# Kernel tuning notes

Hardware: AMD Instinct MI355X
Metric: run time of the kernel (lower is better)

## Reference

```python
import jax, jax.numpy as jnp
import numpy as np


def a_powers(A, t):
    # A: [K, n, n]; returns [t, K, n, n] = stack(I, A, A^2, ..., A^(t-1))
    K, n, _ = A.shape
    result = jnp.broadcast_to(jnp.eye(n, dtype=A.dtype), (1, K, n, n))
    lift = A
    while result.shape[0] < t:
        result = jnp.concatenate([result, result @ lift], axis=0)
        lift = lift @ lift
    return result[:t]


def fast_conv_real(a, b):
    # a: [len1, K, n, n], b: [batch, len2, K, n] -> conv(b, a): [batch, len1+len2-1, K, n]
    len1 = a.shape[0]
    len2 = b.shape[1]
    T = 2 ** int(np.ceil(np.log2(len1 + len2 - 1)))
    Af = jnp.fft.rfft(a, n=T, axis=0)
    Bf = jnp.fft.rfft(b, n=T, axis=1)
    Cf = jnp.einsum('blki,lkij->blkj', Bf, Af)
    c = jnp.fft.irfft(Cf, n=T, axis=1)
    return c[:, :len1 + len2 - 1]


def setup_inputs() -> dict:
    key = jax.random.key(0)
    k_u, k_x0, k_theta, k_B, k_C = jax.random.split(key, 5)
    batch, length = 8, 4096
    input_size, state_size, output_size = 256, 256, 256
    blk = 2
    K = state_size // blk  # 128
    u = jax.random.normal(k_u, (batch, length, input_size), dtype=jnp.float32)
    x0 = jax.random.normal(k_x0, (batch, K, blk), dtype=jnp.float32)
    # A initialized as K random 2x2 rotation blocks (as in __init__)
    theta = 2 * jnp.pi * jax.random.uniform(k_theta, (K,), dtype=jnp.float32)
    c, s = jnp.cos(theta), jnp.sin(theta)
    A = jnp.stack([jnp.stack([c, s], -1), jnp.stack([-s, c], -1)], -2)  # [K, 2, 2]
    B = jax.random.normal(k_B, (input_size, state_size), dtype=jnp.float32) / (state_size + input_size) ** 0.5
    C = jax.random.normal(k_C, (state_size, output_size), dtype=jnp.float32) / (state_size + output_size) ** 0.5
    return {"u": u, "x0": x0, "A": A, "B": B, "C": C}


def reference(u, x0, A, B, C):
    batch, length, _ = u.shape
    K, blk, _ = A.shape
    Aps = a_powers(A, length + 1)          # [length+1, K, blk, blk]
    uB = (u @ B).reshape(batch, length, K, blk)
    x = fast_conv_real(Aps[:-1], uB)[:, :length]  # [batch, length, K, blk]
    x = x + jnp.einsum('bki,lkij->blkj', x0, Aps[1:])
    new_state = x[:, -1]                    # [batch, K, blk]
    y = x.reshape(batch, length, K * blk) @ C
    return (y, new_state)
```

## Files before the change

### kernel.cpp

```cpp
#include <hip/hip_runtime.h>
#include <hip/hip_bf16.h>

typedef __bf16 bf16x2_t __attribute__((ext_vector_type(2)));
typedef __bf16 bf16x8_t __attribute__((ext_vector_type(8)));
typedef float f32x4 __attribute__((ext_vector_type(4)));

#define BATCH   8
#define LENGTH  4096
#define KHALF   128
#define MTOT    (BATCH*LENGTH)
#define NCHUNK  128
#define LC      32

#define SWZ(ch, row) ((ch) ^ ((row) & 7))

__global__ __launch_bounds__(256) void transpose_bc(
    const float* __restrict__ Bsrc, const float* __restrict__ Csrc,
    __bf16* __restrict__ BT, __bf16* __restrict__ CT) {
  const float* src = blockIdx.y ? Csrc : Bsrc;
  __bf16* dst      = blockIdx.y ? CT   : BT;
  int n  = blockIdx.x;
  int kk = threadIdx.x;
  dst[n * 256 + kk] = (__bf16)src[kk * 256 + n];
}

__global__ __launch_bounds__(256) void gemm1_fused(
    const float* __restrict__ u, const __bf16* __restrict__ BT,
    const float* __restrict__ Aarr,
    __bf16* __restrict__ uB, float2* __restrict__ P) {
  __shared__ __align__(16) __bf16 sA[64 * 256];

  const int tid  = threadIdx.x;
  const int lane = tid & 63;
  const int wave = tid >> 6;
  const int m_l  = lane & 15, quad = lane >> 4;
  const int m0   = blockIdx.x * 64;
  const int b    = m0 >> 12;
  const int t0   = m0 & 4095;

#pragma unroll
  for (int i = 0; i < 8; ++i) {
    int s   = tid + i * 256;
    int row = s >> 5, ch = s & 31;
    const float4* g = (const float4*)(u + (size_t)(m0 + row) * 256 + ch * 8);
    float4 a = g[0], c = g[1];
    bf16x8_t v;
    v[0]=(__bf16)a.x; v[1]=(__bf16)a.y; v[2]=(__bf16)a.z; v[3]=(__bf16)a.w;
    v[4]=(__bf16)c.x; v[5]=(__bf16)c.y; v[6]=(__bf16)c.z; v[7]=(__bf16)c.w;
    *(bf16x8_t*)&sA[row * 256 + SWZ(ch, row) * 8] = v;
  }
  __syncthreads();

  f32x4 acc[4][4];
#pragma unroll
  for (int mi = 0; mi < 4; ++mi)
#pragma unroll
    for (int ni = 0; ni < 4; ++ni)
#pragma unroll
      for (int r = 0; r < 4; ++r) acc[mi][ni][r] = 0.f;

#pragma unroll
  for (int kc8 = 0; kc8 < 8; ++kc8) {
    bf16x8_t af[4], bfr[4];
#pragma unroll
    for (int mi = 0; mi < 4; ++mi) {
      int row = mi * 16 + m_l;
      int c   = kc8 * 4 + quad;
      af[mi] = *(const bf16x8_t*)&sA[row * 256 + SWZ(c, row) * 8];
    }
#pragma unroll
    for (int ni = 0; ni < 4; ++ni) {
      int n = wave * 64 + ni * 16 + m_l;
      bfr[ni] = *(const bf16x8_t*)(BT + (size_t)n * 256 + kc8 * 32 + quad * 8);
    }
#pragma unroll
    for (int mi = 0; mi < 4; ++mi)
#pragma unroll
      for (int ni = 0; ni < 4; ++ni)
        acc[mi][ni] = __builtin_amdgcn_mfma_f32_16x16x32_bf16(af[mi], bfr[ni], acc[mi][ni], 0, 0, 0);
  }
  __syncthreads();

  __bf16* sT = sA;
#pragma unroll
  for (int mi = 0; mi < 4; ++mi)
#pragma unroll
    for (int ni = 0; ni < 4; ++ni)
#pragma unroll
      for (int r = 0; r < 4; ++r) {
        int row = mi * 16 + quad * 4 + r;
        int col = wave * 64 + ni * 16 + m_l;
        sT[row * 256 + SWZ(col >> 3, row) * 8 + (col & 7)] = (__bf16)acc[mi][ni][r];
      }
  __syncthreads();

#pragma unroll
  for (int i = 0; i < 8; ++i) {
    int s   = tid + i * 256;
    int row = s >> 5, ch = s & 31;
    *(bf16x8_t*)(uB + (size_t)(m0 + row) * 256 + ch * 8) =
        *(const bf16x8_t*)&sT[row * 256 + SWZ(ch, row) * 8];
  }

  {
    int k   = tid & 127;
    int chl = tid >> 7;
    float cc = Aarr[4 * k], sv = Aarr[4 * k + 1];
    float hr = 0.f, hi = 0.f;
#pragma unroll 8
    for (int j = 0; j < LC; ++j) {
      int row = chl * 32 + j;
      bf16x2_t v2 = *(const bf16x2_t*)&sT[row * 256 + SWZ(k >> 2, row) * 8 + ((2 * k) & 7)];
      float t = fmaf(hr, cc, fmaf(-hi, sv, (float)v2[0]));
      hi      = fmaf(hr, sv, fmaf( hi, cc, (float)v2[1]));
      hr = t;
    }
    int chg = (t0 >> 5) + chl;
    P[((size_t)b * NCHUNK + chg) * KHALF + k] = make_float2(hr, hi);
  }
}

__global__ __launch_bounds__(256) void scan_carry2(
    const float* __restrict__ Aarr, const float* __restrict__ x0,
    const float2* __restrict__ P, float2* __restrict__ H,
    float* __restrict__ state_out) {
  const int lane = threadIdx.x & 63;
  const int wv   = threadIdx.x >> 6;
  const int p    = blockIdx.x * 4 + wv;
  const int b    = p >> 7, k = p & 127;
  const float cc = Aarr[4 * k], sv = Aarr[4 * k + 1];

  float wr = cc, wi = sv;
#pragma unroll
  for (int i = 0; i < 5; ++i) { float nr = wr*wr - wi*wi; wi = 2.f*wr*wi; wr = nr; }
  float Wr[6], Wi[6];
  Wr[0] = wr*wr - wi*wi; Wi[0] = 2.f*wr*wi;
#pragma unroll
  for (int s = 1; s < 6; ++s) { Wr[s] = Wr[s-1]*Wr[s-1] - Wi[s-1]*Wi[s-1]; Wi[s] = 2.f*Wr[s-1]*Wi[s-1]; }

  float2 P0 = P[((size_t)b * NCHUNK + 2 * lane)     * KHALF + k];
  float2 P1 = P[((size_t)b * NCHUNK + 2 * lane + 1) * KHALF + k];
  float qr = fmaf(wr, P0.x, fmaf(-wi, P0.y, P1.x));
  float qi = fmaf(wr, P0.y, fmaf( wi, P0.x, P1.y));
  float Sr = qr, Si = qi;
#pragma unroll
  for (int s = 0; s < 6; ++s) {
    float tr = __shfl_up(Sr, 1 << s, 64);
    float ti = __shfl_up(Si, 1 << s, 64);
    if (lane >= (1 << s)) {
      float nSr = fmaf(Wr[s], tr, fmaf(-Wi[s], ti, Sr));
      float nSi = fmaf(Wr[s], ti, fmaf( Wi[s], tr, Si));
      Sr = nSr; Si = nSi;
    }
  }
  float Ar = __shfl_up(Sr, 1, 64), Ai = __shfl_up(Si, 1, 64);
  if (lane == 0) { Ar = 0.f; Ai = 0.f; }
  float pr = 1.f, pi = 0.f;
#pragma unroll
  for (int s = 0; s < 6; ++s)
    if ((lane >> s) & 1) { float nr = pr*Wr[s] - pi*Wi[s]; pi = pr*Wi[s] + pi*Wr[s]; pr = nr; }

  float x0r = x0[b * 256 + 2 * k], x0i = x0[b * 256 + 2 * k + 1];
  float H0r = fmaf(pr, x0r, fmaf(-pi, x0i, Ar));
  float H0i = fmaf(pr, x0i, fmaf( pi, x0r, Ai));
  H[((size_t)b * NCHUNK + 2 * lane) * KHALF + k] = make_float2(H0r, H0i);
  float H1r = fmaf(wr, H0r, fmaf(-wi, H0i, P0.x));
  float H1i = fmaf(wr, H0i, fmaf( wi, H0r, P0.y));
  H[((size_t)b * NCHUNK + 2 * lane + 1) * KHALF + k] = make_float2(H1r, H1i);
  if (lane == 63) {
    state_out[b * 256 + 2 * k]     = fmaf(wr, H1r, fmaf(-wi, H1i, P1.x));
    state_out[b * 256 + 2 * k + 1] = fmaf(wr, H1i, fmaf( wi, H1r, P1.y));
  }
}

__global__ __launch_bounds__(256) void gemm2_fused(
    const __bf16* __restrict__ uB, const float* __restrict__ Aarr,
    const float2* __restrict__ H, const __bf16* __restrict__ CT,
    float* __restrict__ Y) {
  __shared__ __align__(16) __bf16 sX[64 * 256];

  const int tid  = threadIdx.x;
  const int lane = tid & 63;
  const int wave = tid >> 6;
  const int m_l  = lane & 15, quad = lane >> 4;
  const int m0   = blockIdx.x * 64;
  const int b    = m0 >> 12;
  const int t0   = m0 & 4095;

#pragma unroll
  for (int i = 0; i < 8; ++i) {
    int s   = tid + i * 256;
    int row = s >> 5, ch = s & 31;
    *(bf16x8_t*)&sX[row * 256 + SWZ(ch, row) * 8] =
        *(const bf16x8_t*)(uB + (size_t)(m0 + row) * 256 + ch * 8);
  }
  __syncthreads();

  {
    int k   = tid & 127;
    int chl = tid >> 7;
    float cc = Aarr[4 * k], sv = Aarr[4 * k + 1];
    float2 h = H[((size_t)b * NCHUNK + (t0 >> 5) + chl) * KHALF + k];
    float hr = h.x, hi = h.y;
#pragma unroll 8
    for (int j = 0; j < LC; ++j) {
      int row = chl * 32 + j;
      int idx = row * 256 + SWZ(k >> 2, row) * 8 + ((2 * k) & 7);
      bf16x2_t v2 = *(const bf16x2_t*)&sX[idx];
      float t = fmaf(hr, cc, fmaf(-hi, sv, (float)v2[0]));
      hi      = fmaf(hr, sv, fmaf( hi, cc, (float)v2[1]));
      hr = t;
      bf16x2_t o; o[0] = (__bf16)hr; o[1] = (__bf16)hi;
      *(bf16x2_t*)&sX[idx] = o;
    }
  }
  __syncthreads();

  f32x4 acc[4][4];
#pragma unroll
  for (int mi = 0; mi < 4; ++mi)
#pragma unroll
    for (int ni = 0; ni < 4; ++ni)
#pragma unroll
      for (int r = 0; r < 4; ++r) acc[mi][ni][r] = 0.f;

#pragma unroll
  for (int kc8 = 0; kc8 < 8; ++kc8) {
    bf16x8_t af[4], bfr[4];
#pragma unroll
    for (int mi = 0; mi < 4; ++mi) {
      int row = mi * 16 + m_l;
      int c   = kc8 * 4 + quad;
      af[mi] = *(const bf16x8_t*)&sX[row * 256 + SWZ(c, row) * 8];
    }
#pragma unroll
    for (int ni = 0; ni < 4; ++ni) {
      int n = wave * 64 + ni * 16 + m_l;
      bfr[ni] = *(const bf16x8_t*)(CT + (size_t)n * 256 + kc8 * 32 + quad * 8);
    }
#pragma unroll
    for (int mi = 0; mi < 4; ++mi)
#pragma unroll
      for (int ni = 0; ni < 4; ++ni)
        acc[mi][ni] = __builtin_amdgcn_mfma_f32_16x16x32_bf16(af[mi], bfr[ni], acc[mi][ni], 0, 0, 0);
  }

#pragma unroll
  for (int mi = 0; mi < 4; ++mi)
#pragma unroll
    for (int ni = 0; ni < 4; ++ni)
#pragma unroll
      for (int r = 0; r < 4; ++r) {
        int row = m0 + mi * 16 + quad * 4 + r;
        int col = wave * 64 + ni * 16 + m_l;
        Y[(size_t)row * 256 + col] = acc[mi][ni][r];
      }
}

extern "C" void kernel_launch(void* const* d_in, const int* in_sizes, int n_in,
                              void* d_out, int out_size, void* d_ws, size_t ws_size,
                              hipStream_t stream) {
  const float* u  = (const float*)d_in[0];
  const float* x0 = (const float*)d_in[1];
  const float* A  = (const float*)d_in[2];
  const float* B  = (const float*)d_in[3];
  const float* C  = (const float*)d_in[4];

  float* y         = (float*)d_out;
  float* state_out = y + (size_t)MTOT * 256;

  char* ws = (char*)d_ws;
  __bf16* BT = (__bf16*)ws;  ws += 256 * 256 * 2;
  __bf16* CT = (__bf16*)ws;  ws += 256 * 256 * 2;
  __bf16* uB = (__bf16*)ws;  ws += (size_t)MTOT * 256 * 2;
  float2* P  = (float2*)ws;  ws += (size_t)BATCH * NCHUNK * KHALF * sizeof(float2);
  float2* H  = (float2*)ws;  ws += (size_t)BATCH * NCHUNK * KHALF * sizeof(float2);

  transpose_bc<<<dim3(256, 2), 256, 0, stream>>>(B, C, BT, CT);
  gemm1_fused<<<dim3(MTOT / 64), 256, 0, stream>>>(u, BT, A, uB, P);
  scan_carry2<<<dim3(256), 256, 0, stream>>>(A, x0, P, H, state_out);
  gemm2_fused<<<dim3(MTOT / 64), 256, 0, stream>>>(uB, A, H, CT, y);
}
```

Baseline: 119.2 us.

## Fuse chunk-carry scan into gemm2 by serially recomputing each chunk's prefix

Drops the separate scan_carry2 kernel and the H buffer. Each gemm2_fused thread now rebuilds its chunk's starting state by stepping from x0 through every preceding chunk partial in P, using A^32. The thread on the final chunk also writes new_state. This saves one kernel launch and the H write/read round trip. In exchange, each thread runs a serial loop of up to 127 dependent complex FMAs and P loads, which adds a lot of redundant L2 traffic and latency before the GEMM starts.

```diff
diff --git a/kernel.cpp b/kernel.cpp
--- a/kernel.cpp
+++ b/kernel.cpp
@@ -120,63 +120,11 @@
   }
 }
 
-__global__ __launch_bounds__(256) void scan_carry2(
-    const float* __restrict__ Aarr, const float* __restrict__ x0,
-    const float2* __restrict__ P, float2* __restrict__ H,
-    float* __restrict__ state_out) {
-  const int lane = threadIdx.x & 63;
-  const int wv   = threadIdx.x >> 6;
-  const int p    = blockIdx.x * 4 + wv;
-  const int b    = p >> 7, k = p & 127;
-  const float cc = Aarr[4 * k], sv = Aarr[4 * k + 1];
-
-  float wr = cc, wi = sv;
-#pragma unroll
-  for (int i = 0; i < 5; ++i) { float nr = wr*wr - wi*wi; wi = 2.f*wr*wi; wr = nr; }
-  float Wr[6], Wi[6];
-  Wr[0] = wr*wr - wi*wi; Wi[0] = 2.f*wr*wi;
-#pragma unroll
-  for (int s = 1; s < 6; ++s) { Wr[s] = Wr[s-1]*Wr[s-1] - Wi[s-1]*Wi[s-1]; Wi[s] = 2.f*Wr[s-1]*Wi[s-1]; }
-
-  float2 P0 = P[((size_t)b * NCHUNK + 2 * lane)     * KHALF + k];
-  float2 P1 = P[((size_t)b * NCHUNK + 2 * lane + 1) * KHALF + k];
-  float qr = fmaf(wr, P0.x, fmaf(-wi, P0.y, P1.x));
-  float qi = fmaf(wr, P0.y, fmaf( wi, P0.x, P1.y));
-  float Sr = qr, Si = qi;
-#pragma unroll
-  for (int s = 0; s < 6; ++s) {
-    float tr = __shfl_up(Sr, 1 << s, 64);
-    float ti = __shfl_up(Si, 1 << s, 64);
-    if (lane >= (1 << s)) {
-      float nSr = fmaf(Wr[s], tr, fmaf(-Wi[s], ti, Sr));
-      float nSi = fmaf(Wr[s], ti, fmaf( Wi[s], tr, Si));
-      Sr = nSr; Si = nSi;
-    }
-  }
-  float Ar = __shfl_up(Sr, 1, 64), Ai = __shfl_up(Si, 1, 64);
-  if (lane == 0) { Ar = 0.f; Ai = 0.f; }
-  float pr = 1.f, pi = 0.f;
-#pragma unroll
-  for (int s = 0; s < 6; ++s)
-    if ((lane >> s) & 1) { float nr = pr*Wr[s] - pi*Wi[s]; pi = pr*Wi[s] + pi*Wr[s]; pr = nr; }
-
-  float x0r = x0[b * 256 + 2 * k], x0i = x0[b * 256 + 2 * k + 1];
-  float H0r = fmaf(pr, x0r, fmaf(-pi, x0i, Ar));
-  float H0i = fmaf(pr, x0i, fmaf( pi, x0r, Ai));
-  H[((size_t)b * NCHUNK + 2 * lane) * KHALF + k] = make_float2(H0r, H0i);
-  float H1r = fmaf(wr, H0r, fmaf(-wi, H0i, P0.x));
-  float H1i = fmaf(wr, H0i, fmaf( wi, H0r, P0.y));
-  H[((size_t)b * NCHUNK + 2 * lane + 1) * KHALF + k] = make_float2(H1r, H1i);
-  if (lane == 63) {
-    state_out[b * 256 + 2 * k]     = fmaf(wr, H1r, fmaf(-wi, H1i, P1.x));
-    state_out[b * 256 + 2 * k + 1] = fmaf(wr, H1i, fmaf( wi, H1r, P1.y));
-  }
-}
-
 __global__ __launch_bounds__(256) void gemm2_fused(
     const __bf16* __restrict__ uB, const float* __restrict__ Aarr,
-    const float2* __restrict__ H, const __bf16* __restrict__ CT,
-    float* __restrict__ Y) {
+    const float2* __restrict__ P, const float* __restrict__ x0,
+    const __bf16* __restrict__ CT, float* __restrict__ Y,
+    float* __restrict__ state_out) {
   __shared__ __align__(16) __bf16 sX[64 * 256];
 
   const int tid  = threadIdx.x;
@@ -199,9 +147,21 @@
   {
     int k   = tid & 127;
     int chl = tid >> 7;
+    int chg = (t0 >> 5) + chl;
     float cc = Aarr[4 * k], sv = Aarr[4 * k + 1];
-    float2 h = H[((size_t)b * NCHUNK + (t0 >> 5) + chl) * KHALF + k];
-    float hr = h.x, hi = h.y;
+
+    float wr = cc, wi = sv;
+#pragma unroll
+    for (int i = 0; i < 5; ++i) { float nr = wr*wr - wi*wi; wi = 2.f*wr*wi; wr = nr; }
+
+    float hr = x0[b * 256 + 2 * k], hi = x0[b * 256 + 2 * k + 1];
+    for (int j = 0; j < chg; ++j) {
+      float2 pj = P[((size_t)b * NCHUNK + j) * KHALF + k];
+      float t = fmaf(wr, hr, fmaf(-wi, hi, pj.x));
+      hi      = fmaf(wr, hi, fmaf( wi, hr, pj.y));
+      hr = t;
+    }
+
 #pragma unroll 8
     for (int j = 0; j < LC; ++j) {
       int row = chl * 32 + j;
@@ -213,6 +173,11 @@
       bf16x2_t o; o[0] = (__bf16)hr; o[1] = (__bf16)hi;
       *(bf16x2_t*)&sX[idx] = o;
     }
+
+    if (chg == NCHUNK - 1) {
+      state_out[b * 256 + 2 * k]     = hr;
+      state_out[b * 256 + 2 * k + 1] = hi;
+    }
   }
   __syncthreads();
 
@@ -274,10 +239,8 @@
   __bf16* CT = (__bf16*)ws;  ws += 256 * 256 * 2;
   __bf16* uB = (__bf16*)ws;  ws += (size_t)MTOT * 256 * 2;
   float2* P  = (float2*)ws;  ws += (size_t)BATCH * NCHUNK * KHALF * sizeof(float2);
-  float2* H  = (float2*)ws;  ws += (size_t)BATCH * NCHUNK * KHALF * sizeof(float2);
 
   transpose_bc<<<dim3(256, 2), 256, 0, stream>>>(B, C, BT, CT);
   gemm1_fused<<<dim3(MTOT / 64), 256, 0, stream>>>(u, BT, A, uB, P);
-  scan_carry2<<<dim3(256), 256, 0, stream>>>(A, x0, P, H, state_out);
-  gemm2_fused<<<dim3(MTOT / 64), 256, 0, stream>>>(uB, A, H, CT, y);
-}
+  gemm2_fused<<<dim3(MTOT / 64), 256, 0, stream>>>(uB, A, P, x0, CT, y, state_out);
+}
```

Measured after the change: 144.0 us. 1.21x slower.
